# Optimization experiments

Hardware: AMD Instinct MI355X
Metric: run time of the kernel (lower is better)

Reference implementation:

```python
import jax, jax.numpy as jnp
import numpy as np

EPS = 1e-6
HEADS, HEAD_DIM = 8, 64

def rms_norm_ch(x, g):
    # x: [B,C,H,W], normalize over channel dim, scale g: [C]
    mean = jnp.mean(x * x, axis=1, keepdims=True)
    return x * jax.lax.rsqrt(mean + EPS) * g[None, :, None, None]

def rms_norm_last(x, g):
    # x: [B,L,D], normalize over feature dim, scale g: [D]
    mean = jnp.mean(x * x, axis=-1, keepdims=True)
    return x * jax.lax.rsqrt(mean + EPS) * g

def setup_inputs() -> dict:
    key = jax.random.key(0)
    ks = jax.random.split(key, 5)
    B, C, H, W = 8, 512, 32, 32
    Lc = 1024
    hidden = HEADS * HEAD_DIM  # 512
    x = jax.random.normal(ks[0], (B, C, H, W), dtype=jnp.float32)
    context = jax.random.normal(ks[1], (B, Lc, C), dtype=jnp.float32)
    Wq = jax.random.normal(ks[2], (hidden, C), dtype=jnp.float32) * 0.02
    Wkv = jax.random.normal(ks[3], (2 * hidden, C), dtype=jnp.float32) * 0.02
    Wo = jax.random.normal(ks[4], (C, hidden), dtype=jnp.float32) * 0.02
    bo = jnp.zeros((C,), dtype=jnp.float32)
    g = jnp.ones((C,), dtype=jnp.float32)   # shared RMSNorm scale (pre-attn)
    g2 = jnp.ones((C,), dtype=jnp.float32)  # output RMSNorm scale
    return {"x": x, "context": context, "Wq": Wq, "Wkv": Wkv, "Wo": Wo, "bo": bo, "g": g, "g2": g2}

def reference(x, context, Wq, Wkv, Wo, bo, g, g2):
    B, C, H, W = x.shape
    Lc = context.shape[1]
    hidden = HEADS * HEAD_DIM
    scale = HEAD_DIM ** -0.5

    # Q projection: 1x1 conv == per-pixel matmul
    xn = rms_norm_ch(x, g)
    q = jnp.einsum('oc,bchw->bohw', Wq, xn)                     # [B,hidden,H,W]
    q = q.reshape(B, HEADS, HEAD_DIM, H * W) * scale            # [B,h,d,lw1]

    # K,V from context tokens
    cn = rms_norm_last(context, g)
    kv = jnp.einsum('bld,od->blo', cn, Wkv)                     # [B,Lc,2*hidden]
    k, v = jnp.split(kv, 2, axis=-1)
    k = k.reshape(B, Lc, HEADS, HEAD_DIM).transpose(0, 2, 3, 1)  # [B,h,d,lw2]
    v = v.reshape(B, Lc, HEADS, HEAD_DIM).transpose(0, 2, 3, 1)  # [B,h,d,lw2]

    sim = jnp.einsum('bhci,bhcj->bhij', q, k)                   # [B,h,lw1,lw2]
    attn = jax.nn.softmax(sim, axis=-1)
    out = jnp.einsum('bhij,bhcj->bhic', attn, v)                # [B,h,lw1,d]

    out = out.transpose(0, 1, 3, 2).reshape(B, hidden, H, W)    # b (h c) l w
    y = jnp.einsum('oc,bchw->bohw', Wo, out) + bo[None, :, None, None]
    y = rms_norm_ch(y, g2)
    return y + x
```

## Files before the change

kernel.cpp:

```cpp
#include <hip/hip_runtime.h>
#include <hip/hip_bf16.h>

using bf16 = __hip_bfloat16;
typedef float f32x4 __attribute__((ext_vector_type(4)));
typedef short s16x8 __attribute__((ext_vector_type(8)));
typedef short s16x4 __attribute__((ext_vector_type(4)));

#define B_N   8
#define C_N   512
#define HW_N  1024
#define LC_N  1024
#define HID_N 512
#define NHEAD 8
#define DHEAD 64
#define EPSN  1e-6f

__device__ __forceinline__ f32x4 mfma16(s16x8 a, s16x8 b, f32x4 c) {
  return __builtin_amdgcn_mfma_f32_16x16x32_bf16(a, b, c, 0, 0, 0);
}
__device__ __forceinline__ void gload_lds16(const void* g, void* l) {
  __builtin_amdgcn_global_load_lds((const __attribute__((address_space(1))) void*)g,
                                   (__attribute__((address_space(3))) void*)l, 16, 0, 0);
}
__device__ __forceinline__ s16x8 ld8(const bf16* p) {
  return *reinterpret_cast<const s16x8*>(p);
}
__device__ __forceinline__ unsigned short bfbits(float f) {
  return __builtin_bit_cast(unsigned short, __float2bfloat16(f));
}

__global__ __launch_bounds__(256) void prep_weights(
    const float* __restrict__ Wq, const float* __restrict__ Wkv,
    const float* __restrict__ Wo, const float* __restrict__ g,
    bf16* __restrict__ Wqg, bf16* __restrict__ Wkvg, bf16* __restrict__ Wob,
    float* __restrict__ ssqx, float* __restrict__ ssqy)
{
  int idx = blockIdx.x * 256 + threadIdx.x;
  const int NQ = 512 * 512, NKV = 1024 * 512;
  if (idx < 8192) { ssqx[idx] = 0.f; ssqy[idx] = 0.f; }
  if (idx < NQ) {
    Wqg[idx] = __float2bfloat16(Wq[idx] * g[idx & 511]);
  } else if (idx < NQ + NKV) {
    int j = idx - NQ;
    Wkvg[j] = __float2bfloat16(Wkv[j] * g[j & 511]);
  } else {
    int j = idx - NQ - NKV;
    Wob[j] = __float2bfloat16(Wo[j]);
  }
}

__global__ __launch_bounds__(256) void xbf_kernel(
    const float* __restrict__ x, bf16* __restrict__ xbf, float* __restrict__ ssqx)
{
  __shared__ float tile[32][33];
  __shared__ float part[8][32];
  int b = blockIdx.z, c0 = blockIdx.y * 32, p0 = blockIdx.x * 32;
  int tx = threadIdx.x & 31, ty = threadIdx.x >> 5;
#pragma unroll
  for (int j = 0; j < 4; ++j) {
    int c = ty + j * 8;
    tile[c][tx] = x[((long)b * C_N + c0 + c) * HW_N + p0 + tx];
  }
  __syncthreads();
  {
    float s = 0.f;
#pragma unroll
    for (int i = 0; i < 4; ++i) {
      float v = tile[ty * 4 + i][tx];
      s += v * v;
    }
    part[ty][tx] = s;
  }
#pragma unroll
  for (int j = 0; j < 4; ++j) {
    int p = ty + j * 8;
    xbf[((long)b * HW_N + p0 + p) * C_N + c0 + tx] = __float2bfloat16(tile[tx][p]);
  }
  __syncthreads();
  if (ty == 0) {
    float tot = 0.f;
#pragma unroll
    for (int i = 0; i < 8; ++i) tot += part[i][tx];
    atomicAdd(&ssqx[b * HW_N + p0 + tx], tot);
  }
}

__global__ __launch_bounds__(256) void ctxnorm_kernel(
    const float* __restrict__ ctx, bf16* __restrict__ cnbf)
{
  int row = blockIdx.x * 4 + (threadIdx.x >> 6);
  int lane = threadIdx.x & 63;
  const float* cr = ctx + (long)row * C_N;
  float4 v0 = ((const float4*)cr)[lane * 2];
  float4 v1 = ((const float4*)cr)[lane * 2 + 1];
  float s = v0.x*v0.x + v0.y*v0.y + v0.z*v0.z + v0.w*v0.w
          + v1.x*v1.x + v1.y*v1.y + v1.z*v1.z + v1.w*v1.w;
#pragma unroll
  for (int m = 1; m < 64; m <<= 1) s += __shfl_xor(s, m);
  float r = rsqrtf(s * (1.0f / C_N) + EPSN);
  bf16 tmp[8];
  tmp[0] = __float2bfloat16(v0.x * r); tmp[1] = __float2bfloat16(v0.y * r);
  tmp[2] = __float2bfloat16(v0.z * r); tmp[3] = __float2bfloat16(v0.w * r);
  tmp[4] = __float2bfloat16(v1.x * r); tmp[5] = __float2bfloat16(v1.y * r);
  tmp[6] = __float2bfloat16(v1.z * r); tmp[7] = __float2bfloat16(v1.w * r);
  *reinterpret_cast<s16x8*>(cnbf + (long)row * C_N + lane * 8) =
      *reinterpret_cast<const s16x8*>(tmp);
}

__device__ __forceinline__ void gemm128_core(
    const bf16* __restrict__ A, const bf16* __restrict__ W, int K, int m0, int n0,
    bf16* __restrict__ sA, bf16* __restrict__ sB, f32x4 (&acc)[4][4])
{
  const int t = threadIdx.x;
  const int lane = t & 63, w = t >> 6;
  const int wm = (w >> 1) * 64, wn = (w & 1) * 64;
  const int lr = lane & 15, hi = lane >> 4;
  const int r = t >> 2, seg = t & 3;
  const long aoff0 = (long)(m0 + r) * K + seg * 8;
  const long aoff1 = (long)(m0 + 64 + r) * K + seg * 8;
  const long woff0 = (long)(n0 + r) * K + seg * 8;
  const long woff1 = (long)(n0 + 64 + r) * K + seg * 8;
  const int d0 = r * 32 + seg * 8, d1 = (64 + r) * 32 + seg * 8;

#define GSTAGE(buf, k0)                                           \
  do {                                                            \
    gload_lds16(A + aoff0 + (k0), &sA[(buf) * 4096 + d0]);        \
    gload_lds16(A + aoff1 + (k0), &sA[(buf) * 4096 + d1]);        \
    gload_lds16(W + woff0 + (k0), &sB[(buf) * 4096 + d0]);        \
    gload_lds16(W + woff1 + (k0), &sB[(buf) * 4096 + d1]);        \
  } while (0)

  GSTAGE(0, 0);
  __syncthreads();
  int cur = 0;
  for (int k0 = 0; k0 < K; k0 += 32) {
    if (k0 + 32 < K) GSTAGE(cur ^ 1, k0 + 32);
    s16x8 af[4], bfr[4];
#pragma unroll
    for (int mi = 0; mi < 4; ++mi)
      af[mi] = *reinterpret_cast<const s16x8*>(
          &sA[cur * 4096 + (wm + mi * 16 + lr) * 32 + hi * 8]);
#pragma unroll
    for (int ni = 0; ni < 4; ++ni)
      bfr[ni] = *reinterpret_cast<const s16x8*>(
          &sB[cur * 4096 + (wn + ni * 16 + lr) * 32 + hi * 8]);
    __builtin_amdgcn_s_setprio(1);
#pragma unroll
    for (int mi = 0; mi < 4; ++mi)
#pragma unroll
      for (int ni = 0; ni < 4; ++ni)
        acc[mi][ni] = mfma16(af[mi], bfr[ni], acc[mi][ni]);
    __builtin_amdgcn_s_setprio(0);
    __syncthreads();
    cur ^= 1;
  }
#undef GSTAGE
}

__global__ __launch_bounds__(256, 2)
void gemm_qkv(const bf16* __restrict__ xbf, const bf16* __restrict__ cnbf,
              const bf16* __restrict__ Wqg, const bf16* __restrict__ Wkvg,
              const float* __restrict__ ssqx,
              bf16* __restrict__ qbf, bf16* __restrict__ kvbf, bf16* __restrict__ vT)
{
  __shared__ bf16 sA[2 * 4096];
  __shared__ bf16 sB[2 * 4096];
  const int bid = blockIdx.x;
  const bf16 *A, *W;
  int m0, n0;
  bool isQ;
  if (bid < 256) {
    isQ = true;  A = xbf;  W = Wqg;
    m0 = (bid >> 2) * 128; n0 = (bid & 3) * 128;
  } else {
    isQ = false; A = cnbf; W = Wkvg;
    int b2 = bid - 256;
    m0 = (b2 >> 3) * 128; n0 = (b2 & 7) * 128;
  }
  f32x4 acc[4][4] = {};
  gemm128_core(A, W, C_N, m0, n0, sA, sB, acc);

  const int lane = threadIdx.x & 63, w = threadIdx.x >> 6;
  const int wm = (w >> 1) * 64, wn = (w & 1) * 64;
  const int lr = lane & 15, hi = lane >> 4;
#pragma unroll
  for (int mi = 0; mi < 4; ++mi) {
#pragma unroll
    for (int rr = 0; rr < 4; ++rr) {
      int row = m0 + wm + mi * 16 + hi * 4 + rr;
      float rsc = 0.f;
      if (isQ)
        rsc = rsqrtf(ssqx[row] * (1.0f / C_N) + EPSN) * 0.18033688011112042f;
#pragma unroll
      for (int ni = 0; ni < 4; ++ni) {
        int col = n0 + wn + ni * 16 + lr;
        float v = acc[mi][ni][rr];
        if (isQ) {
          qbf[(long)row * HID_N + col] = __float2bfloat16(v * rsc);
        } else if (col < HID_N) {
          kvbf[(long)row * (2 * HID_N) + col] = __float2bfloat16(v);
        } else {
          int b = row >> 10, l = row & 1023;
          vT[((long)b * HID_N + (col - HID_N)) * LC_N + l] = __float2bfloat16(v);
        }
      }
    }
  }
}

__global__ __launch_bounds__(256, 2)
void gemm_o(const bf16* __restrict__ attno, const bf16* __restrict__ Wob,
            const float* __restrict__ bo, float* __restrict__ ytmp,
            float* __restrict__ ssqy)
{
  __shared__ bf16 sA[2 * 4096];
  __shared__ bf16 sB[2 * 4096];
  const int m0 = (blockIdx.x >> 2) * 128;
  const int n0 = (blockIdx.x & 3) * 128;
  f32x4 acc[4][4] = {};
  gemm128_core(attno, Wob, HID_N, m0, n0, sA, sB, acc);

  const int lane = threadIdx.x & 63, w = threadIdx.x >> 6;
  const int wm = (w >> 1) * 64, wn = (w & 1) * 64;
  const int lr = lane & 15, hi = lane >> 4;
  float ss[4][4];
#pragma unroll
  for (int mi = 0; mi < 4; ++mi)
#pragma unroll
    for (int rr = 0; rr < 4; ++rr) ss[mi][rr] = 0.f;

#pragma unroll
  for (int mi = 0; mi < 4; ++mi) {
#pragma unroll
    for (int ni = 0; ni < 4; ++ni) {
      float bb = bo[n0 + wn + ni * 16 + lr];
#pragma unroll
      for (int rr = 0; rr < 4; ++rr) {
        int row = m0 + wm + mi * 16 + hi * 4 + rr;
        int col = n0 + wn + ni * 16 + lr;
        float v = acc[mi][ni][rr] + bb;
        ytmp[(long)row * C_N + col] = v;
        ss[mi][rr] += v * v;
      }
    }
  }
#pragma unroll
  for (int mi = 0; mi < 4; ++mi)
#pragma unroll
    for (int rr = 0; rr < 4; ++rr) {
      float s = ss[mi][rr];
      s += __shfl_xor(s, 1); s += __shfl_xor(s, 2);
      s += __shfl_xor(s, 4); s += __shfl_xor(s, 8);
      if (lr == 0) atomicAdd(&ssqy[m0 + wm + mi * 16 + hi * 4 + rr], s);
    }
}

__global__ __launch_bounds__(256, 2)
void attn_fused(const bf16* __restrict__ qbf, const bf16* __restrict__ kvbf,
                const bf16* __restrict__ vT, bf16* __restrict__ attno)
{
  __shared__ bf16 sK[2][4096];
  __shared__ bf16 sV[2][4096];
  __shared__ bf16 Pl[4][32 * 72];
  const int t = threadIdx.x;
  const int wv = t >> 6, lane = t & 63;
  const int lr = lane & 15, hi = lane >> 4;
  const int hi8 = hi * 8, hi4 = hi * 4;
  const int bh = blockIdx.x, b = bh >> 3, h = bh & 7;
  const int q_base = blockIdx.y * 128 + wv * 32;

  const bf16* kbase = kvbf + (long)b * LC_N * 1024 + h * DHEAD;
  const bf16* vbase = vT + ((long)b * HID_N + h * DHEAD) * (long)LC_N;
  bf16* Pw = Pl[wv];

  s16x8 qf[2][2];
#pragma unroll
  for (int qt = 0; qt < 2; ++qt)
#pragma unroll
    for (int c = 0; c < 2; ++c)
      qf[qt][c] = ld8(qbf + ((long)b * HW_N + q_base + qt * 16 + lr) * HID_N
                          + h * DHEAD + c * 32 + hi8);

  const int srow = lane >> 2;
  const int scol = (lane & 3) * 8;

#define ASTAGE(buf, l0n)                                                        \
  do {                                                                          \
    _Pragma("unroll")                                                           \
    for (int j = 0; j < 4; ++j) {                                               \
      int lin = wv * 4 + j;                                                     \
      int cc = (lin >> 2) & 1, qq = lin & 3;                                    \
      if (lin < 8) {                                                            \
        gload_lds16(kbase + (long)((l0n) + qq * 16 + srow) * 1024 + cc * 32 + scol, \
                    &sK[buf][cc * 2048 + qq * 512 + lane * 8]);                 \
      } else {                                                                  \
        gload_lds16(vbase + (long)(qq * 16 + srow) * 1024 + (l0n) + cc * 32 + scol, \
                    &sV[buf][cc * 2048 + qq * 512 + lane * 8]);                 \
      }                                                                         \
    }                                                                           \
  } while (0)

  float m[2] = {-1e30f, -1e30f};
  float lsum[2] = {0.f, 0.f};
  f32x4 o[2][4] = {};

  ASTAGE(0, 0);
  __syncthreads();
  int cur = 0;

#pragma unroll 1
  for (int l0 = 0; l0 < LC_N; l0 += 64) {
    if (l0 + 64 < LC_N) ASTAGE(cur ^ 1, l0 + 64);

    f32x4 st[4][2] = {};
    __builtin_amdgcn_s_setprio(1);
#pragma unroll
    for (int kt = 0; kt < 4; ++kt) {
      s16x8 k0 = *reinterpret_cast<const s16x8*>(&sK[cur][(kt * 16 + lr) * 32 + hi8]);
      s16x8 k1 = *reinterpret_cast<const s16x8*>(&sK[cur][2048 + (kt * 16 + lr) * 32 + hi8]);
      st[kt][0] = mfma16(k0, qf[0][0], st[kt][0]);
      st[kt][0] = mfma16(k1, qf[0][1], st[kt][0]);
      st[kt][1] = mfma16(k0, qf[1][0], st[kt][1]);
      st[kt][1] = mfma16(k1, qf[1][1], st[kt][1]);
    }
    __builtin_amdgcn_s_setprio(0);

    float pmax[2];
#pragma unroll
    for (int qt = 0; qt < 2; ++qt) {
      float mx = st[0][qt][0];
#pragma unroll
      for (int kt = 0; kt < 4; ++kt)
#pragma unroll
        for (int rr = 0; rr < 4; ++rr)
          mx = fmaxf(mx, st[kt][qt][rr]);
      pmax[qt] = mx;
    }
    bool ok = (pmax[0] <= m[0] + 8.f) && (pmax[1] <= m[1] + 8.f);
    if (!__all(ok)) {
#pragma unroll
      for (int qt = 0; qt < 2; ++qt) {
        float rm = pmax[qt];
        rm = fmaxf(rm, __shfl_xor(rm, 16));
        rm = fmaxf(rm, __shfl_xor(rm, 32));
        float mn = fmaxf(m[qt], rm);
        float al = __builtin_amdgcn_exp2f(m[qt] - mn);
        m[qt] = mn;
        lsum[qt] *= al;
        float arr[4];
#pragma unroll
        for (int rr = 0; rr < 4; ++rr) arr[rr] = __shfl(al, hi4 + rr);
#pragma unroll
        for (int dt = 0; dt < 4; ++dt)
#pragma unroll
          for (int rr = 0; rr < 4; ++rr) o[qt][dt][rr] *= arr[rr];
      }
    }

#pragma unroll
    for (int qt = 0; qt < 2; ++qt) {
      float ls = 0.f;
#pragma unroll
      for (int kt = 0; kt < 4; ++kt) {
        float p0 = __builtin_amdgcn_exp2f(st[kt][qt][0] - m[qt]);
        float p1 = __builtin_amdgcn_exp2f(st[kt][qt][1] - m[qt]);
        float p2 = __builtin_amdgcn_exp2f(st[kt][qt][2] - m[qt]);
        float p3 = __builtin_amdgcn_exp2f(st[kt][qt][3] - m[qt]);
        ls += (p0 + p1) + (p2 + p3);
        s16x4 pk;
        pk[0] = (short)bfbits(p0); pk[1] = (short)bfbits(p1);
        pk[2] = (short)bfbits(p2); pk[3] = (short)bfbits(p3);
        *reinterpret_cast<s16x4*>(&Pw[(qt * 16 + lr) * 72 + kt * 16 + hi4]) = pk;
      }
      lsum[qt] += ls;
    }

    __builtin_amdgcn_s_setprio(1);
#pragma unroll
    for (int c = 0; c < 2; ++c) {
      s16x8 pa0 = *reinterpret_cast<const s16x8*>(&Pw[(0 * 16 + lr) * 72 + c * 32 + hi8]);
      s16x8 pa1 = *reinterpret_cast<const s16x8*>(&Pw[(1 * 16 + lr) * 72 + c * 32 + hi8]);
#pragma unroll
      for (int dt = 0; dt < 4; ++dt) {
        s16x8 vv = *reinterpret_cast<const s16x8*>(
            &sV[cur][c * 2048 + (dt * 16 + lr) * 32 + hi8]);
        o[0][dt] = mfma16(pa0, vv, o[0][dt]);
        o[1][dt] = mfma16(pa1, vv, o[1][dt]);
      }
    }
    __builtin_amdgcn_s_setprio(0);

    __syncthreads();
    cur ^= 1;
  }
#undef ASTAGE

#pragma unroll
  for (int qt = 0; qt < 2; ++qt) {
    float ls = lsum[qt];
    ls += __shfl_xor(ls, 16);
    ls += __shfl_xor(ls, 32);
    float linv[4];
#pragma unroll
    for (int rr = 0; rr < 4; ++rr) linv[rr] = 1.f / __shfl(ls, hi4 + rr);
#pragma unroll
    for (int dt = 0; dt < 4; ++dt)
#pragma unroll
      for (int rr = 0; rr < 4; ++rr)
        attno[((long)b * HW_N + q_base + qt * 16 + hi4 + rr) * HID_N
              + h * DHEAD + dt * 16 + lr] = __float2bfloat16(o[qt][dt][rr] * linv[rr]);
  }
}

__global__ __launch_bounds__(256) void final_kernel(
    const float* __restrict__ ytmp, const float* __restrict__ g2,
    const float* __restrict__ ssqy, const float* __restrict__ x,
    float* __restrict__ out)
{
  __shared__ float tile[32][33];
  int b = blockIdx.z, c0 = blockIdx.y * 32, p0 = blockIdx.x * 32;
  int tx = threadIdx.x & 31, ty = threadIdx.x >> 5;
#pragma unroll
  for (int j = 0; j < 4; ++j) {
    int p = ty + j * 8;
    tile[p][tx] = ytmp[((long)b * HW_N + p0 + p) * C_N + c0 + tx];
  }
  __syncthreads();
  float r = rsqrtf(ssqy[b * HW_N + p0 + tx] * (1.0f / C_N) + EPSN);
#pragma unroll
  for (int j = 0; j < 4; ++j) {
    int c = ty + j * 8;
    long oidx = ((long)b * C_N + c0 + c) * HW_N + p0 + tx;
    out[oidx] = tile[tx][c] * r * g2[c0 + c] + x[oidx];
  }
}

extern "C" void kernel_launch(void* const* d_in, const int* in_sizes, int n_in,
                              void* d_out, int out_size, void* d_ws, size_t ws_size,
                              hipStream_t stream) {
  const float* x   = (const float*)d_in[0];
  const float* ctx = (const float*)d_in[1];
  const float* Wq  = (const float*)d_in[2];
  const float* Wkv = (const float*)d_in[3];
  const float* Wo  = (const float*)d_in[4];
  const float* bo  = (const float*)d_in[5];
  const float* g   = (const float*)d_in[6];
  const float* g2  = (const float*)d_in[7];
  float* out = (float*)d_out;

  char* ws = (char*)d_ws;
  bf16*  Wqg   = (bf16*)(ws + 0);
  bf16*  Wkvg  = (bf16*)(ws + 524288);
  bf16*  Wob   = (bf16*)(ws + 1572864);
  float* ssqx  = (float*)(ws + 2097152);
  float* ssqy  = (float*)(ws + 2129920);
  bf16*  xbf   = (bf16*)(ws + 2162688);
  bf16*  cnbf  = (bf16*)(ws + 10551296);
  bf16*  qbf   = (bf16*)(ws + 18939904);
  bf16*  kvbf  = (bf16*)(ws + 27328512);
  bf16*  vT    = (bf16*)(ws + 44105728);
  bf16*  attno = (bf16*)(ws + 52494336);
  float* ytmp  = (float*)(ws + 2162688);

  prep_weights<<<4096, 256, 0, stream>>>(Wq, Wkv, Wo, g, Wqg, Wkvg, Wob, ssqx, ssqy);
  xbf_kernel<<<dim3(32, 16, 8), 256, 0, stream>>>(x, xbf, ssqx);
  ctxnorm_kernel<<<2048, 256, 0, stream>>>(ctx, cnbf);

  gemm_qkv<<<768, 256, 0, stream>>>(xbf, cnbf, Wqg, Wkvg, ssqx, qbf, kvbf, vT);

  attn_fused<<<dim3(64, 8), 256, 0, stream>>>(qbf, kvbf, vT, attno);

  gemm_o<<<256, 256, 0, stream>>>(attno, Wob, bo, ytmp, ssqy);

  final_kernel<<<dim3(32, 16, 8), 256, 0, stream>>>(ytmp, g2, ssqy, x, out);
}
```

Baseline: 184.9 us.

## Swizzle LDS tiles, merge preprocessing kernels, and vectorize V-transpose stores

XOR-swizzles the 16-byte segment index in the LDS tiles of the GEMM core and the attention K/V staging, so the MFMA fragment reads avoid bank conflicts. The weight conversion, x transpose/ssq, and context norm kernels are merged into one launch, with a small separate kernel that zeroes the accumulators. The QKV epilogue now branches per block instead of per element and writes vT as packed 4-element stores. These reduce launch count, LDS conflicts and scattered 2-byte writes, but the merged kernel carries a larger shared-memory footprint for every block.

```diff
diff --git a/kernel.cpp b/kernel.cpp
--- a/kernel.cpp
+++ b/kernel.cpp
@@ -11,7 +11,6 @@
 #define HW_N  1024
 #define LC_N  1024
 #define HID_N 512
-#define NHEAD 8
 #define DHEAD 64
 #define EPSN  1e-6f
 
@@ -29,98 +28,105 @@
   return __builtin_bit_cast(unsigned short, __float2bfloat16(f));
 }
 
-__global__ __launch_bounds__(256) void prep_weights(
+__global__ __launch_bounds__(256) void init_kernel(
+    float* __restrict__ ssqx, float* __restrict__ ssqy)
+{
+  int i = blockIdx.x * 256 + threadIdx.x;
+  if (i < 8192) { ssqx[i] = 0.f; ssqy[i] = 0.f; }
+}
+
+__global__ __launch_bounds__(256) void pre_kernel(
+    const float* __restrict__ x, const float* __restrict__ ctx,
     const float* __restrict__ Wq, const float* __restrict__ Wkv,
     const float* __restrict__ Wo, const float* __restrict__ g,
     bf16* __restrict__ Wqg, bf16* __restrict__ Wkvg, bf16* __restrict__ Wob,
-    float* __restrict__ ssqx, float* __restrict__ ssqy)
-{
-  int idx = blockIdx.x * 256 + threadIdx.x;
-  const int NQ = 512 * 512, NKV = 1024 * 512;
-  if (idx < 8192) { ssqx[idx] = 0.f; ssqy[idx] = 0.f; }
-  if (idx < NQ) {
-    Wqg[idx] = __float2bfloat16(Wq[idx] * g[idx & 511]);
-  } else if (idx < NQ + NKV) {
-    int j = idx - NQ;
-    Wkvg[j] = __float2bfloat16(Wkv[j] * g[j & 511]);
+    bf16* __restrict__ xbf, bf16* __restrict__ cnbf, float* __restrict__ ssqx)
+{
+  __shared__ float sm[1056 + 256];
+  const int bid = blockIdx.x, tid = threadIdx.x;
+
+  if (bid < 4096) {
+    int idx = bid * 256 + tid;
+    const int NQ = 512 * 512, NKV = 1024 * 512;
+    if (idx < NQ) {
+      Wqg[idx] = __float2bfloat16(Wq[idx] * g[idx & 511]);
+    } else if (idx < NQ + NKV) {
+      int j = idx - NQ;
+      Wkvg[j] = __float2bfloat16(Wkv[j] * g[j & 511]);
+    } else {
+      int j = idx - NQ - NKV;
+      Wob[j] = __float2bfloat16(Wo[j]);
+    }
+  } else if (bid < 8192) {
+    float* tile = sm;
+    float* part = sm + 1056;
+    int t = bid - 4096;
+    int b = t >> 9, c0 = ((t >> 5) & 15) * 32, p0 = (t & 31) * 32;
+    int tx = tid & 31, ty = tid >> 5;
+#pragma unroll
+    for (int j = 0; j < 4; ++j) {
+      int c = ty + j * 8;
+      tile[c * 33 + tx] = x[((long)b * C_N + c0 + c) * HW_N + p0 + tx];
+    }
+    __syncthreads();
+    {
+      float s = 0.f;
+#pragma unroll
+      for (int i = 0; i < 4; ++i) {
+        float v = tile[(ty * 4 + i) * 33 + tx];
+        s += v * v;
+      }
+      part[ty * 32 + tx] = s;
+    }
+#pragma unroll
+    for (int j = 0; j < 4; ++j) {
+      int p = ty + j * 8;
+      xbf[((long)b * HW_N + p0 + p) * C_N + c0 + tx] = __float2bfloat16(tile[tx * 33 + p]);
+    }
+    __syncthreads();
+    if (ty == 0) {
+      float tot = 0.f;
+#pragma unroll
+      for (int i = 0; i < 8; ++i) tot += part[i * 32 + tx];
+      atomicAdd(&ssqx[b * HW_N + p0 + tx], tot);
+    }
   } else {
-    int j = idx - NQ - NKV;
-    Wob[j] = __float2bfloat16(Wo[j]);
-  }
-}
-
-__global__ __launch_bounds__(256) void xbf_kernel(
-    const float* __restrict__ x, bf16* __restrict__ xbf, float* __restrict__ ssqx)
-{
-  __shared__ float tile[32][33];
-  __shared__ float part[8][32];
-  int b = blockIdx.z, c0 = blockIdx.y * 32, p0 = blockIdx.x * 32;
-  int tx = threadIdx.x & 31, ty = threadIdx.x >> 5;
-#pragma unroll
-  for (int j = 0; j < 4; ++j) {
-    int c = ty + j * 8;
-    tile[c][tx] = x[((long)b * C_N + c0 + c) * HW_N + p0 + tx];
-  }
-  __syncthreads();
-  {
-    float s = 0.f;
-#pragma unroll
-    for (int i = 0; i < 4; ++i) {
-      float v = tile[ty * 4 + i][tx];
-      s += v * v;
-    }
-    part[ty][tx] = s;
-  }
-#pragma unroll
-  for (int j = 0; j < 4; ++j) {
-    int p = ty + j * 8;
-    xbf[((long)b * HW_N + p0 + p) * C_N + c0 + tx] = __float2bfloat16(tile[tx][p]);
-  }
-  __syncthreads();
-  if (ty == 0) {
-    float tot = 0.f;
-#pragma unroll
-    for (int i = 0; i < 8; ++i) tot += part[i][tx];
-    atomicAdd(&ssqx[b * HW_N + p0 + tx], tot);
-  }
-}
-
-__global__ __launch_bounds__(256) void ctxnorm_kernel(
-    const float* __restrict__ ctx, bf16* __restrict__ cnbf)
-{
-  int row = blockIdx.x * 4 + (threadIdx.x >> 6);
-  int lane = threadIdx.x & 63;
-  const float* cr = ctx + (long)row * C_N;
-  float4 v0 = ((const float4*)cr)[lane * 2];
-  float4 v1 = ((const float4*)cr)[lane * 2 + 1];
-  float s = v0.x*v0.x + v0.y*v0.y + v0.z*v0.z + v0.w*v0.w
-          + v1.x*v1.x + v1.y*v1.y + v1.z*v1.z + v1.w*v1.w;
-#pragma unroll
-  for (int m = 1; m < 64; m <<= 1) s += __shfl_xor(s, m);
-  float r = rsqrtf(s * (1.0f / C_N) + EPSN);
-  bf16 tmp[8];
-  tmp[0] = __float2bfloat16(v0.x * r); tmp[1] = __float2bfloat16(v0.y * r);
-  tmp[2] = __float2bfloat16(v0.z * r); tmp[3] = __float2bfloat16(v0.w * r);
-  tmp[4] = __float2bfloat16(v1.x * r); tmp[5] = __float2bfloat16(v1.y * r);
-  tmp[6] = __float2bfloat16(v1.z * r); tmp[7] = __float2bfloat16(v1.w * r);
-  *reinterpret_cast<s16x8*>(cnbf + (long)row * C_N + lane * 8) =
-      *reinterpret_cast<const s16x8*>(tmp);
+    int row = (bid - 8192) * 4 + (tid >> 6);
+    int lane = tid & 63;
+    const float* cr = ctx + (long)row * C_N;
+    float4 v0 = ((const float4*)cr)[lane * 2];
+    float4 v1 = ((const float4*)cr)[lane * 2 + 1];
+    float s = v0.x*v0.x + v0.y*v0.y + v0.z*v0.z + v0.w*v0.w
+            + v1.x*v1.x + v1.y*v1.y + v1.z*v1.z + v1.w*v1.w;
+#pragma unroll
+    for (int m = 1; m < 64; m <<= 1) s += __shfl_xor(s, m);
+    float r = rsqrtf(s * (1.0f / C_N) + EPSN);
+    bf16 tmp[8];
+    tmp[0] = __float2bfloat16(v0.x * r); tmp[1] = __float2bfloat16(v0.y * r);
+    tmp[2] = __float2bfloat16(v0.z * r); tmp[3] = __float2bfloat16(v0.w * r);
+    tmp[4] = __float2bfloat16(v1.x * r); tmp[5] = __float2bfloat16(v1.y * r);
+    tmp[6] = __float2bfloat16(v1.z * r); tmp[7] = __float2bfloat16(v1.w * r);
+    *reinterpret_cast<s16x8*>(cnbf + (long)row * C_N + lane * 8) =
+        *reinterpret_cast<const s16x8*>(tmp);
+  }
 }
 
 __device__ __forceinline__ void gemm128_core(
     const bf16* __restrict__ A, const bf16* __restrict__ W, int K, int m0, int n0,
-    bf16* __restrict__ sA, bf16* __restrict__ sB, f32x4 (&acc)[4][4])
+    bf16* sA, bf16* sB, f32x4 (&acc)[4][4])
 {
   const int t = threadIdx.x;
   const int lane = t & 63, w = t >> 6;
   const int wm = (w >> 1) * 64, wn = (w & 1) * 64;
   const int lr = lane & 15, hi = lane >> 4;
   const int r = t >> 2, seg = t & 3;
-  const long aoff0 = (long)(m0 + r) * K + seg * 8;
-  const long aoff1 = (long)(m0 + 64 + r) * K + seg * 8;
-  const long woff0 = (long)(n0 + r) * K + seg * 8;
-  const long woff1 = (long)(n0 + 64 + r) * K + seg * 8;
+  const int segsw = seg ^ ((r >> 1) & 3);
+  const long aoff0 = (long)(m0 + r) * K + segsw * 8;
+  const long aoff1 = (long)(m0 + 64 + r) * K + segsw * 8;
+  const long woff0 = (long)(n0 + r) * K + segsw * 8;
+  const long woff1 = (long)(n0 + 64 + r) * K + segsw * 8;
   const int d0 = r * 32 + seg * 8, d1 = (64 + r) * 32 + seg * 8;
+  const int kofs = (hi ^ ((lr >> 1) & 3)) * 8;
 
 #define GSTAGE(buf, k0)                                           \
   do {                                                            \
@@ -139,11 +145,11 @@
 #pragma unroll
     for (int mi = 0; mi < 4; ++mi)
       af[mi] = *reinterpret_cast<const s16x8*>(
-          &sA[cur * 4096 + (wm + mi * 16 + lr) * 32 + hi * 8]);
+          &sA[cur * 4096 + (wm + mi * 16 + lr) * 32 + kofs]);
 #pragma unroll
     for (int ni = 0; ni < 4; ++ni)
       bfr[ni] = *reinterpret_cast<const s16x8*>(
-          &sB[cur * 4096 + (wn + ni * 16 + lr) * 32 + hi * 8]);
+          &sB[cur * 4096 + (wn + ni * 16 + lr) * 32 + kofs]);
     __builtin_amdgcn_s_setprio(1);
 #pragma unroll
     for (int mi = 0; mi < 4; ++mi)
@@ -183,76 +189,49 @@
   const int lane = threadIdx.x & 63, w = threadIdx.x >> 6;
   const int wm = (w >> 1) * 64, wn = (w & 1) * 64;
   const int lr = lane & 15, hi = lane >> 4;
-#pragma unroll
-  for (int mi = 0; mi < 4; ++mi) {
-#pragma unroll
-    for (int rr = 0; rr < 4; ++rr) {
-      int row = m0 + wm + mi * 16 + hi * 4 + rr;
-      float rsc = 0.f;
-      if (isQ)
-        rsc = rsqrtf(ssqx[row] * (1.0f / C_N) + EPSN) * 0.18033688011112042f;
-#pragma unroll
-      for (int ni = 0; ni < 4; ++ni) {
-        int col = n0 + wn + ni * 16 + lr;
-        float v = acc[mi][ni][rr];
-        if (isQ) {
-          qbf[(long)row * HID_N + col] = __float2bfloat16(v * rsc);
-        } else if (col < HID_N) {
-          kvbf[(long)row * (2 * HID_N) + col] = __float2bfloat16(v);
-        } else {
-          int b = row >> 10, l = row & 1023;
-          vT[((long)b * HID_N + (col - HID_N)) * LC_N + l] = __float2bfloat16(v);
-        }
-      }
-    }
-  }
-}
-
-__global__ __launch_bounds__(256, 2)
-void gemm_o(const bf16* __restrict__ attno, const bf16* __restrict__ Wob,
-            const float* __restrict__ bo, float* __restrict__ ytmp,
-            float* __restrict__ ssqy)
-{
-  __shared__ bf16 sA[2 * 4096];
-  __shared__ bf16 sB[2 * 4096];
-  const int m0 = (blockIdx.x >> 2) * 128;
-  const int n0 = (blockIdx.x & 3) * 128;
-  f32x4 acc[4][4] = {};
-  gemm128_core(attno, Wob, HID_N, m0, n0, sA, sB, acc);
-
-  const int lane = threadIdx.x & 63, w = threadIdx.x >> 6;
-  const int wm = (w >> 1) * 64, wn = (w & 1) * 64;
-  const int lr = lane & 15, hi = lane >> 4;
-  float ss[4][4];
-#pragma unroll
-  for (int mi = 0; mi < 4; ++mi)
-#pragma unroll
-    for (int rr = 0; rr < 4; ++rr) ss[mi][rr] = 0.f;
-
-#pragma unroll
-  for (int mi = 0; mi < 4; ++mi) {
-#pragma unroll
-    for (int ni = 0; ni < 4; ++ni) {
-      float bb = bo[n0 + wn + ni * 16 + lr];
+
+  if (isQ) {
+#pragma unroll
+    for (int mi = 0; mi < 4; ++mi) {
 #pragma unroll
       for (int rr = 0; rr < 4; ++rr) {
         int row = m0 + wm + mi * 16 + hi * 4 + rr;
-        int col = n0 + wn + ni * 16 + lr;
-        float v = acc[mi][ni][rr] + bb;
-        ytmp[(long)row * C_N + col] = v;
-        ss[mi][rr] += v * v;
-      }
-    }
-  }
-#pragma unroll
-  for (int mi = 0; mi < 4; ++mi)
-#pragma unroll
-    for (int rr = 0; rr < 4; ++rr) {
-      float s = ss[mi][rr];
-      s += __shfl_xor(s, 1); s += __shfl_xor(s, 2);
-      s += __shfl_xor(s, 4); s += __shfl_xor(s, 8);
-      if (lr == 0) atomicAdd(&ssqy[m0 + wm + mi * 16 + hi * 4 + rr], s);
-    }
+        float rsc = rsqrtf(ssqx[row] * (1.0f / C_N) + EPSN) * 0.18033688011112042f;
+#pragma unroll
+        for (int ni = 0; ni < 4; ++ni) {
+          int col = n0 + wn + ni * 16 + lr;
+          qbf[(long)row * HID_N + col] = __float2bfloat16(acc[mi][ni][rr] * rsc);
+        }
+      }
+    }
+  } else if (n0 < HID_N) {
+#pragma unroll
+    for (int mi = 0; mi < 4; ++mi)
+#pragma unroll
+      for (int rr = 0; rr < 4; ++rr) {
+        int row = m0 + wm + mi * 16 + hi * 4 + rr;
+#pragma unroll
+        for (int ni = 0; ni < 4; ++ni) {
+          int col = n0 + wn + ni * 16 + lr;
+          kvbf[(long)row * (2 * HID_N) + col] = __float2bfloat16(acc[mi][ni][rr]);
+        }
+      }
+  } else {
+    const int bq = m0 >> 10;
+    const int l0 = (m0 & 1023) + wm;
+#pragma unroll
+    for (int mi = 0; mi < 4; ++mi) {
+#pragma unroll
+      for (int ni = 0; ni < 4; ++ni) {
+        int d = n0 - HID_N + wn + ni * 16 + lr;
+        s16x4 pk;
+#pragma unroll
+        for (int rr = 0; rr < 4; ++rr) pk[rr] = (short)bfbits(acc[mi][ni][rr]);
+        *reinterpret_cast<s16x4*>(
+            &vT[((long)(bq * HID_N + d)) * LC_N + l0 + mi * 16 + hi * 4]) = pk;
+      }
+    }
+  }
 }
 
 __global__ __launch_bounds__(256, 2)
@@ -282,7 +261,8 @@
                           + h * DHEAD + c * 32 + hi8);
 
   const int srow = lane >> 2;
-  const int scol = (lane & 3) * 8;
+  const int scol = ((lane & 3) ^ ((lane >> 3) & 3)) * 8;
+  const int rxofs = (hi ^ ((lr >> 1) & 3)) * 8;
 
 #define ASTAGE(buf, l0n)                                                        \
   do {                                                                          \
@@ -316,8 +296,8 @@
     __builtin_amdgcn_s_setprio(1);
 #pragma unroll
     for (int kt = 0; kt < 4; ++kt) {
-      s16x8 k0 = *reinterpret_cast<const s16x8*>(&sK[cur][(kt * 16 + lr) * 32 + hi8]);
-      s16x8 k1 = *reinterpret_cast<const s16x8*>(&sK[cur][2048 + (kt * 16 + lr) * 32 + hi8]);
+      s16x8 k0 = *reinterpret_cast<const s16x8*>(&sK[cur][(kt * 16 + lr) * 32 + rxofs]);
+      s16x8 k1 = *reinterpret_cast<const s16x8*>(&sK[cur][2048 + (kt * 16 + lr) * 32 + rxofs]);
       st[kt][0] = mfma16(k0, qf[0][0], st[kt][0]);
       st[kt][0] = mfma16(k1, qf[0][1], st[kt][0]);
       st[kt][1] = mfma16(k0, qf[1][0], st[kt][1]);
@@ -383,7 +363,7 @@
 #pragma unroll
       for (int dt = 0; dt < 4; ++dt) {
         s16x8 vv = *reinterpret_cast<const s16x8*>(
-            &sV[cur][c * 2048 + (dt * 16 + lr) * 32 + hi8]);
+            &sV[cur][c * 2048 + (dt * 16 + lr) * 32 + rxofs]);
         o[0][dt] = mfma16(pa0, vv, o[0][dt]);
         o[1][dt] = mfma16(pa1, vv, o[1][dt]);
       }
@@ -412,18 +392,66 @@
   }
 }
 
+__global__ __launch_bounds__(256, 2)
+void gemm_o(const bf16* __restrict__ attno, const bf16* __restrict__ Wob,
+            const float* __restrict__ bo, float* __restrict__ ytmp,
+            float* __restrict__ ssqy)
+{
+  __shared__ bf16 sA[2 * 4096];
+  __shared__ bf16 sB[2 * 4096];
+  const int m0 = (blockIdx.x >> 2) * 128;
+  const int n0 = (blockIdx.x & 3) * 128;
+  f32x4 acc[4][4] = {};
+  gemm128_core(attno, Wob, HID_N, m0, n0, sA, sB, acc);
+
+  const int lane = threadIdx.x & 63, w = threadIdx.x >> 6;
+  const int wm = (w >> 1) * 64, wn = (w & 1) * 64;
+  const int lr = lane & 15, hi = lane >> 4;
+  float ss[4][4];
+#pragma unroll
+  for (int mi = 0; mi < 4; ++mi)
+#pragma unroll
+    for (int rr = 0; rr < 4; ++rr) ss[mi][rr] = 0.f;
+
+#pragma unroll
+  for (int mi = 0; mi < 4; ++mi) {
+#pragma unroll
+    for (int ni = 0; ni < 4; ++ni) {
+      float bb = bo[n0 + wn + ni * 16 + lr];
+#pragma unroll
+      for (int rr = 0; rr < 4; ++rr) {
+        int row = m0 + wm + mi * 16 + hi * 4 + rr;
+        int col = n0 + wn + ni * 16 + lr;
+        float v = acc[mi][ni][rr] + bb;
+        ytmp[(long)row * C_N + col] = v;
+        ss[mi][rr] += v * v;
+      }
+    }
+  }
+#pragma unroll
+  for (int mi = 0; mi < 4; ++mi)
+#pragma unroll
+    for (int rr = 0; rr < 4; ++rr) {
+      float s = ss[mi][rr];
+      s += __shfl_xor(s, 1); s += __shfl_xor(s, 2);
+      s += __shfl_xor(s, 4); s += __shfl_xor(s, 8);
+      if (lr == 0) atomicAdd(&ssqy[m0 + wm + mi * 16 + hi * 4 + rr], s);
+    }
+}
+
 __global__ __launch_bounds__(256) void final_kernel(
     const float* __restrict__ ytmp, const float* __restrict__ g2,
     const float* __restrict__ ssqy, const float* __restrict__ x,
     float* __restrict__ out)
 {
-  __shared__ float tile[32][33];
-  int b = blockIdx.z, c0 = blockIdx.y * 32, p0 = blockIdx.x * 32;
+  __shared__ float tile[32 * 33];
+  const int t = blockIdx.x;
+  int b = t >> 9, c0 = ((t >> 5) & 15) * 32, p0 = (t & 31) * 32;
   int tx = threadIdx.x & 31, ty = threadIdx.x >> 5;
 #pragma unroll
   for (int j = 0; j < 4; ++j) {
     int p = ty + j * 8;
-    tile[p][tx] = ytmp[((long)b * HW_N + p0 + p) * C_N + c0 + tx];
+    tile[p * 33 + tx] = ytmp[((long)b * HW_N + p0 + p) * C_N + c0 + tx];
   }
   __syncthreads();
   float r = rsqrtf(ssqy[b * HW_N + p0 + tx] * (1.0f / C_N) + EPSN);
@@ -431,7 +459,7 @@
   for (int j = 0; j < 4; ++j) {
     int c = ty + j * 8;
     long oidx = ((long)b * C_N + c0 + c) * HW_N + p0 + tx;
-    out[oidx] = tile[tx][c] * r * g2[c0 + c] + x[oidx];
+    out[oidx] = tile[tx * 33 + c] * r * g2[c0 + c] + x[oidx];
   }
 }
 
@@ -462,15 +490,11 @@
   bf16*  attno = (bf16*)(ws + 52494336);
   float* ytmp  = (float*)(ws + 2162688);
 
-  prep_weights<<<4096, 256, 0, stream>>>(Wq, Wkv, Wo, g, Wqg, Wkvg, Wob, ssqx, ssqy);
-  xbf_kernel<<<dim3(32, 16, 8), 256, 0, stream>>>(x, xbf, ssqx);
-  ctxnorm_kernel<<<2048, 256, 0, stream>>>(ctx, cnbf);
-
+  init_kernel<<<32, 256, 0, stream>>>(ssqx, ssqy);
+  pre_kernel<<<10240, 256, 0, stream>>>(x, ctx, Wq, Wkv, Wo, g,
+                                        Wqg, Wkvg, Wob, xbf, cnbf, ssqx);
   gemm_qkv<<<768, 256, 0, stream>>>(xbf, cnbf, Wqg, Wkvg, ssqx, qbf, kvbf, vT);
-
   attn_fused<<<dim3(64, 8), 256, 0, stream>>>(qbf, kvbf, vT, attno);
-
   gemm_o<<<256, 256, 0, stream>>>(attno, Wob, bo, ytmp, ssqy);
-
-  final_kernel<<<dim3(32, 16, 8), 256, 0, stream>>>(ytmp, g2, ssqy, x, out);
-}
+  final_kernel<<<4096, 256, 0, stream>>>(ytmp, g2, ssqy, x, out);
+}
```

Result: faster. 170.3 us (-7.9%).
